# Performance work log

Hardware: AMD Instinct MI355X
Metric: run time of the kernel (lower is better)

Reference implementation:

```python
import jax, jax.numpy as jnp
import numpy as np

D_MODEL = 1024
NUM_HEADS = 16
HEAD_DIM = D_MODEL // NUM_HEADS
ROPE_BASE = 10000.0


def _rotate_half(x):
    x1, x2 = jnp.split(x, 2, axis=-1)
    return jnp.concatenate([-x2, x1], axis=-1)


def _rope_cache(seq_len, head_dim, dtype):
    half = head_dim // 2
    inv_freq = 1.0 / (ROPE_BASE ** (jnp.arange(half, dtype=jnp.float32) / float(half)))
    t = jnp.arange(seq_len, dtype=jnp.float32)
    freqs = t[:, None] * inv_freq[None, :]          # [s, half]
    emb = jnp.concatenate([freqs, freqs], axis=-1)   # [s, head_dim]
    cos = jnp.cos(emb)[None, None, :, :].astype(dtype)  # [1,1,s,d]
    sin = jnp.sin(emb)[None, None, :, :].astype(dtype)
    return cos, sin


def setup_inputs() -> dict:
    key = jax.random.key(0)
    k1, k2, k3 = jax.random.split(key, 3)
    b, s = 4, 2048
    x = jax.random.normal(k1, (b, s, D_MODEL), dtype=jnp.float32)
    mask = jnp.ones((b, s), dtype=jnp.float32)
    Wqkv = jax.random.normal(k2, (D_MODEL, 3 * D_MODEL), dtype=jnp.float32) * (D_MODEL ** -0.5)
    Wout = jax.random.normal(k3, (D_MODEL, D_MODEL), dtype=jnp.float32) * (D_MODEL ** -0.5)
    return {"x": x, "mask": mask, "Wqkv": Wqkv, "Wout": Wout}


def reference(x, mask, Wqkv, Wout):
    b, s, _ = x.shape
    qkv = x @ Wqkv                                   # [b,s,3*d_model]
    q, k, v = jnp.split(qkv, 3, axis=-1)

    def split_heads(t):
        return t.reshape(b, s, NUM_HEADS, HEAD_DIM).transpose(0, 2, 1, 3)  # [b,h,s,d]

    q, k, v = map(split_heads, (q, k, v))
    cos, sin = _rope_cache(s, HEAD_DIM, x.dtype)
    q = q * cos + _rotate_half(q) * sin
    k = k * cos + _rotate_half(k) * sin

    scale = HEAD_DIM ** -0.5
    logits = jnp.einsum('bhid,bhjd->bhij', q, k) * scale
    logits = logits + (1.0 - mask)[:, None, None, :] * -1e9
    attn = jax.nn.softmax(logits, axis=-1)
    out = jnp.einsum('bhij,bhjd->bhid', attn, v)     # [b,h,s,d]
    out = out.transpose(0, 2, 1, 3).reshape(b, s, D_MODEL)
    return out @ Wout
```

## Files before the change

### kernel.cpp

```cpp
#include <hip/hip_runtime.h>

typedef unsigned short u16;
typedef unsigned int u32;
typedef int i32x2 __attribute__((ext_vector_type(2)));
typedef float f32x4 __attribute__((ext_vector_type(4)));
typedef float f32x16 __attribute__((ext_vector_type(16)));
typedef __bf16 bf16x8 __attribute__((ext_vector_type(8)));
typedef unsigned short u16x8 __attribute__((ext_vector_type(8)));
typedef unsigned short u16x4 __attribute__((ext_vector_type(4)));
typedef unsigned int u32x4 __attribute__((ext_vector_type(4)));

#define S_ 2048
#define DM 1024

#define LDS_U32(p) ((__attribute__((address_space(3))) unsigned int*)(p))
#define GLB_U32(p) ((const __attribute__((address_space(1))) unsigned int*)(p))

__device__ __forceinline__ u16 f2bf(float f) {
    unsigned int u = __float_as_uint(f);
    u += 0x7fffu + ((u >> 16) & 1u);
    return (u16)(u >> 16);
}
__device__ __forceinline__ float bf2f(u16 s) {
    return __uint_as_float(((unsigned int)s) << 16);
}
__device__ __forceinline__ float fast_exp2(float x) {
#if __has_builtin(__builtin_amdgcn_exp2f)
    return __builtin_amdgcn_exp2f(x);
#else
    return __expf(x * 0.69314718056f);
#endif
}

__global__ __launch_bounds__(256) void f32_to_bf16_kernel(const float* __restrict__ in,
                                                          u16* __restrict__ o, int n) {
    int i = (blockIdx.x * 256 + threadIdx.x) << 2;
    if (i >= n) return;
    float4 f = *(const float4*)&in[i];
    u16x4 r;
    r[0] = f2bf(f.x); r[1] = f2bf(f.y); r[2] = f2bf(f.z); r[3] = f2bf(f.w);
    *(u16x4*)&o[i] = r;
}

__global__ __launch_bounds__(256) void transpose_w(const float* __restrict__ W,
                                                   u16* __restrict__ Wt, int K, int N) {
    __shared__ float tile[32][33];
    int nb = blockIdx.x << 5, kb = blockIdx.y << 5;
    int tx = threadIdx.x & 31, ty = threadIdx.x >> 5;
#pragma unroll
    for (int r = 0; r < 32; r += 8)
        tile[ty + r][tx] = W[(size_t)(kb + ty + r) * N + nb + tx];
    __syncthreads();
#pragma unroll
    for (int r = 0; r < 32; r += 8)
        Wt[(size_t)(nb + ty + r) * K + kb + tx] = f2bf(tile[tx][ty + r]);
}


#define ABLK(B, KK) ((B) * 24576 + (KK) * 4096)
#define BBLK(B, KK) ((B) * 24576 + 8192 + (KK) * 8192)

template <int MODE>
__global__ __launch_bounds__(512, 1) void gemm256(const u16* __restrict__ A,
                                                  const u16* __restrict__ Bt,
                                                  float* __restrict__ Cf,
                                                  u16* __restrict__ Qp, u16* __restrict__ Kp,
                                                  u16* __restrict__ Vtp,
                                                  int M, int N, int K) {
    __shared__ __align__(16) u16 lds[73728];
    const int tid = threadIdx.x, wave = tid >> 6, lane = tid & 63;
    const int Ntiles = N >> 8;
    const int cpx = gridDim.x >> 3;
    const int bid = (int)blockIdx.x;
    const int wg = (bid & 7) * cpx + (bid >> 3);
    const int mt = wg / Ntiles, nt = wg % Ntiles;
    const int m0 = mt << 7, n0 = nt << 8;
    const int wm = (wave >> 2) << 6, wn = (wave & 3) << 6;
    const int lr = lane & 15, lu = lane >> 4;

    const int NT = K >> 6;

    f32x4 acc[4][4] = {};

    const int srow0 = wave * 16 + (lane >> 2);
    const int scole = (((lane & 3) ^ ((lane >> 3) & 3)) << 3);

#define STAGE_A(BLK, KCOL)                                                                \
    {                                                                                     \
        const u16* src = &A[(size_t)(m0 + srow0) * K + (KCOL) + scole];                   \
        __builtin_amdgcn_global_load_lds(GLB_U32(src),                                    \
            LDS_U32(&lds[(BLK) + wave * 512]), 16, 0, 0);                                 \
    }
#define STAGE_B(BLK, KCOL)                                                                \
    {                                                                                     \
        _Pragma("unroll") for (int l = 0; l < 2; ++l) {                                   \
            const u16* src = &Bt[(size_t)(n0 + srow0 + l * 128) * K + (KCOL) + scole];    \
            __builtin_amdgcn_global_load_lds(GLB_U32(src),                                \
                LDS_U32(&lds[(BLK) + l * 4096 + wave * 512]), 16, 0, 0);                  \
        }                                                                                 \
    }

#define LDFRAG(BLK, ROW) \
    __builtin_bit_cast(bf16x8, *(const u16x8*)&lds[(BLK) + (ROW) * 32 + ((lu ^ (((ROW) >> 1) & 3)) << 3)])

#define PHASE(BUF, KK, SBUF, SKK, SKT)                                                    \
    {                                                                                     \
        _Pragma("unroll") for (int ii = 0; ii < 4; ++ii)                                  \
            af[ii] = LDFRAG(ABLK(BUF, KK), wm + ii * 16 + lr);                            \
        _Pragma("unroll") for (int j = 0; j < 4; ++j)                                     \
            bfv[j] = LDFRAG(BBLK(BUF, KK), wn + j * 16 + lr);                             \
        {                                                                                 \
            const int kcol = (((SKT) & (NT - 1)) << 6) + ((SKK) << 5);                    \
            STAGE_A(ABLK(SBUF, SKK), kcol);                                               \
            STAGE_B(BBLK(SBUF, SKK), kcol);                                               \
        }                                                                                 \
        asm volatile("s_barrier" ::: "memory");                                           \
        asm volatile("s_waitcnt lgkmcnt(0)" ::: "memory");                                \
        __builtin_amdgcn_sched_barrier(0);                                                \
        __builtin_amdgcn_s_setprio(1);                                                    \
        _Pragma("unroll") for (int ii = 0; ii < 4; ++ii)                                  \
            _Pragma("unroll") for (int j = 0; j < 4; ++j)                                 \
                acc[ii][j] = __builtin_amdgcn_mfma_f32_16x16x32_bf16(                     \
                    af[ii], bfv[j], acc[ii][j], 0, 0, 0);                                 \
        __builtin_amdgcn_s_setprio(0);                                                    \
        asm volatile("s_waitcnt vmcnt(9)" ::: "memory");                                  \
        asm volatile("s_barrier" ::: "memory");                                           \
    }

    STAGE_A(ABLK(0, 0), 0);
    STAGE_B(BBLK(0, 0), 0);
    STAGE_A(ABLK(0, 1), 32);
    STAGE_B(BBLK(0, 1), 32);
    STAGE_A(ABLK(1, 0), 64);
    STAGE_B(BBLK(1, 0), 64);
    STAGE_A(ABLK(1, 1), 96);
    STAGE_B(BBLK(1, 1), 96);
    asm volatile("s_waitcnt vmcnt(9)" ::: "memory");
    asm volatile("s_barrier" ::: "memory");

    int bt = 0, bs = 2;
    for (int t = 0; t < NT; ++t) {
        bf16x8 af[4], bfv[4];
        const int tn = t + 2;
        PHASE(bt, 0, bs, 0, tn);
        PHASE(bt, 1, bs, 1, tn);
        bt = (bt == 2) ? 0 : bt + 1;
        bs = (bs == 2) ? 0 : bs + 1;
    }

    if (MODE == 0) {
        const int t = (n0 + wn) >> 10;
        if (t < 2) {
            const float LN1E4_32 = 9.210340371976184f / 32.0f;
            const float invf0 = __expf(-(float)lr * LN1E4_32);
            const float invf1 = __expf(-(float)(lr + 16) * LN1E4_32);
#pragma unroll
            for (int i = 0; i < 4; ++i) {
                const int rbase = m0 + wm + (i << 4) + ((lane >> 4) << 2);
#pragma unroll
                for (int jj = 0; jj < 4; ++jj) {
                    const float s = (float)((rbase + jj) & (S_ - 1));
                    float sn0, c0, sn1, c1;
                    __sincosf(s * invf0, &sn0, &c0);
                    __sincosf(s * invf1, &sn1, &c1);
                    const float v0 = acc[i][0][jj], v1 = acc[i][1][jj];
                    const float v2 = acc[i][2][jj], v3 = acc[i][3][jj];
                    acc[i][0][jj] = v0 * c0 - v2 * sn0;
                    acc[i][2][jj] = v2 * c0 + v0 * sn0;
                    acc[i][1][jj] = v1 * c1 - v3 * sn1;
                    acc[i][3][jj] = v3 * c1 + v1 * sn1;
                }
            }
            u16* P = (t == 0) ? Qp : Kp;
#pragma unroll
            for (int i = 0; i < 4; ++i) {
#pragma unroll
                for (int j = 0; j < 4; ++j) {
                    int rbase = m0 + wm + (i << 4) + ((lane >> 4) << 2);
                    int col = n0 + wn + (j << 4) + lr;
                    int h = (col & 1023) >> 6, d = col & 63;
#pragma unroll
                    for (int jj = 0; jj < 4; ++jj) {
                        int row = rbase + jj;
                        int b = row >> 11, s = row & 2047;
                        P[((size_t)((b << 4) + h) * S_ + s) * 64 + d] = f2bf(acc[i][j][jj]);
                    }
                }
            }
        } else {
#pragma unroll
            for (int i = 0; i < 4; ++i) {
                const int rbase = m0 + wm + (i << 4) + ((lane >> 4) << 2);
                const int b = rbase >> 11, sb = rbase & 2047;
#pragma unroll
                for (int j = 0; j < 4; ++j) {
                    int col = n0 + wn + (j << 4) + lr;
                    int h = (col & 1023) >> 6, d = col & 63;
                    u16x4 pk;
#pragma unroll
                    for (int jj = 0; jj < 4; ++jj) pk[jj] = f2bf(acc[i][j][jj]);
                    *(u16x4*)&Vtp[((size_t)((b << 4) + h) * 64 + d) * S_ + sb] = pk;
                }
            }
        }
    } else {
#pragma unroll
        for (int i = 0; i < 4; ++i)
#pragma unroll
            for (int j = 0; j < 4; ++j) {
                int rbase = m0 + wm + (i << 4) + ((lane >> 4) << 2);
                int col = n0 + wn + (j << 4) + lr;
#pragma unroll
                for (int jj = 0; jj < 4; ++jj)
                    Cf[(size_t)(rbase + jj) * N + col] = acc[i][j][jj];
            }
    }
#undef PHASE
#undef LDFRAG
#undef STAGE_B
#undef STAGE_A
}

__device__ __forceinline__ void softmax_chain(f32x16* p, f32x16* acc, f32x16& accS,
                                              float& m_run, u32* wa, u32* wb,
                                              const float* madd_tile, bool hasmask,
                                              float* bcast_w, int c, int hi) {
    if (hasmask) {
#pragma unroll
        for (int tt = 0; tt < 2; ++tt)
#pragma unroll
            for (int rq = 0; rq < 4; ++rq) {
                float4 mf = *(const float4*)&madd_tile[tt * 32 + rq * 8 + hi * 4];
                p[tt][4 * rq + 0] += mf.x;
                p[tt][4 * rq + 1] += mf.y;
                p[tt][4 * rq + 2] += mf.z;
                p[tt][4 * rq + 3] += mf.w;
            }
    }

    float tm[16];
#pragma unroll
    for (int r = 0; r < 16; ++r) tm[r] = fmaxf(p[0][r], p[1][r]);
    float a0 = fmaxf(fmaxf(tm[0], tm[1]), tm[2]);
    float a1 = fmaxf(fmaxf(tm[3], tm[4]), tm[5]);
    float a2 = fmaxf(fmaxf(tm[6], tm[7]), tm[8]);
    float a3 = fmaxf(fmaxf(tm[9], tm[10]), tm[11]);
    float a4 = fmaxf(fmaxf(tm[12], tm[13]), tm[14]);
    float b0 = fmaxf(fmaxf(a0, a1), a2);
    float b1 = fmaxf(fmaxf(a3, a4), tm[15]);
    float mx = fmaxf(b0, b1);
    {
        i32x2 mm = __builtin_amdgcn_permlane32_swap(__float_as_int(mx), __float_as_int(mx), false, false);
        mx = fmaxf(__int_as_float(mm[0]), __int_as_float(mm[1]));
    }

    if (!__all(mx - m_run <= 8.0f)) {
        float mnew = fmaxf(m_run, mx);
        float alpha = fast_exp2(m_run - mnew);
        m_run = mnew;
        bcast_w[c] = alpha;
        float avf[16];
#pragma unroll
        for (int rq = 0; rq < 4; ++rq) {
            float4 t4 = *(const float4*)&bcast_w[rq * 8 + hi * 4];
            avf[4 * rq + 0] = t4.x; avf[4 * rq + 1] = t4.y;
            avf[4 * rq + 2] = t4.z; avf[4 * rq + 3] = t4.w;
        }
#pragma unroll
        for (int r = 0; r < 16; ++r) {
            acc[0][r] *= avf[r];
            acc[1][r] *= avf[r];
            accS[r]   *= avf[r];
        }
    }

#pragma unroll
    for (int tt = 0; tt < 2; ++tt)
#pragma unroll
        for (int r = 0; r < 16; ++r)
            p[tt][r] = fast_exp2(p[tt][r] - m_run);

#pragma unroll
    for (int tt = 0; tt < 2; ++tt)
#pragma unroll
        for (int rq = 0; rq < 4; ++rq) {
            float e0 = p[tt][4 * rq + 0], e1 = p[tt][4 * rq + 1];
            float e2 = p[tt][4 * rq + 2], e3 = p[tt][4 * rq + 3];
            u32 w0, w1;
            asm("v_cvt_pk_bf16_f32 %0, %1, %2" : "=v"(w0) : "v"(e0), "v"(e1));
            asm("v_cvt_pk_bf16_f32 %0, %1, %2" : "=v"(w1) : "v"(e2), "v"(e3));
            wa[4 * tt + rq] = w0;
            wb[4 * tt + rq] = w1;
        }
}

__global__ __launch_bounds__(256, 2) void attn_kernel(const u16* __restrict__ q,
                                                      const u16* __restrict__ k,
                                                      const u16* __restrict__ vt,
                                                      const float* __restrict__ mask,
                                                      u16* __restrict__ outp) {
    __shared__ __align__(16) u16 Kl[2][64 * 64];
    __shared__ __align__(16) u16 Vl[2][64 * 64];
    __shared__ float madd2[2][64];
    __shared__ float bcast[4][32];

    const int tid = threadIdx.x, wave = tid >> 6, lane = tid & 63;
    const int c = lane & 31, hi = lane >> 5, c7 = c & 7;
    const int bh = blockIdx.x & 63, qt = blockIdx.x >> 6;
    const int b = bh >> 4, h = bh & 15;
    const size_t base = (size_t)bh * (S_ * 64);
    const int qrowA = (qt << 8) + (wave << 5) + c;
    const int qrowB = qrowA + 128;

    const float QS = 0.18033688f;

    bf16x8 qfA[4], qfB[4];
#pragma unroll
    for (int j = 0; j < 4; ++j) {
        u16x8 rawA = *(const u16x8*)&q[base + (size_t)qrowA * 64 + j * 16 + hi * 8];
        u16x8 rawB = *(const u16x8*)&q[base + (size_t)qrowB * 64 + j * 16 + hi * 8];
        u16x8 scA, scB;
#pragma unroll
        for (int e = 0; e < 8; ++e) {
            scA[e] = f2bf(bf2f(rawA[e]) * QS);
            scB[e] = f2bf(bf2f(rawB[e]) * QS);
        }
        qfA[j] = __builtin_bit_cast(bf16x8, scA);
        qfB[j] = __builtin_bit_cast(bf16x8, scB);
    }

    u16x8 ou;
#pragma unroll
    for (int e = 0; e < 8; ++e) ou[e] = 0x3F80;
    const bf16x8 onesf = __builtin_bit_cast(bf16x8, ou);

    f32x16 accA[2] = {}, accB[2] = {};
    f32x16 accSA = {}, accSB = {};
    float m_runA = -1e30f, m_runB = -1e30f;

    const int sr = tid >> 2, su = (tid & 3) << 1;
    const int so0 = sr * 64 + ((su ^ (sr & 7)) << 3);
    const int so1 = sr * 64 + (((su + 1) ^ (sr & 7)) << 3);

    u16x8 kc0 = *(const u16x8*)&k[base + (size_t)sr * 64 + su * 8];
    u16x8 kc1 = *(const u16x8*)&k[base + (size_t)sr * 64 + su * 8 + 8];
    u16x8 vc0 = *(const u16x8*)&vt[base + (size_t)sr * S_ + su * 8];
    u16x8 vc1 = *(const u16x8*)&vt[base + (size_t)sr * S_ + su * 8 + 8];
    float mval = (tid < 64) ? mask[b * S_ + tid] : 1.0f;

    for (int t = 0; t < 32; ++t) {
        const int bi = t & 1;
        u16* Kb = &Kl[bi][0];
        u16* Vb = &Vl[bi][0];
        *(u16x8*)&Kb[so0] = kc0;
        *(u16x8*)&Kb[so1] = kc1;
        *(u16x8*)&Vb[so0] = vc0;
        *(u16x8*)&Vb[so1] = vc1;
        if (tid < 64) madd2[bi][tid] = (1.0f - mval) * -1.44269504e9f;
        if (t + 1 < 32) {
            const int kn = (t + 1) << 6;
            kc0 = *(const u16x8*)&k[base + (size_t)(kn + sr) * 64 + su * 8];
            kc1 = *(const u16x8*)&k[base + (size_t)(kn + sr) * 64 + su * 8 + 8];
            vc0 = *(const u16x8*)&vt[base + (size_t)sr * S_ + kn + su * 8];
            vc1 = *(const u16x8*)&vt[base + (size_t)sr * S_ + kn + su * 8 + 8];
            mval = (tid < 64) ? mask[b * S_ + kn + tid] : 1.0f;
        }
        __syncthreads();

        f32x16 pA[2] = {}, pB[2] = {};
        __builtin_amdgcn_s_setprio(1);
#pragma unroll
        for (int j = 0; j < 4; ++j) {
            const int uo = ((2 * j + hi) ^ c7) << 3;
            bf16x8 ka  = __builtin_bit_cast(bf16x8, *(const u16x8*)&Kb[c * 64 + uo]);
            bf16x8 kb2 = __builtin_bit_cast(bf16x8, *(const u16x8*)&Kb[(32 + c) * 64 + uo]);
            pA[0] = __builtin_amdgcn_mfma_f32_32x32x16_bf16(ka,  qfA[j], pA[0], 0, 0, 0);
            pA[1] = __builtin_amdgcn_mfma_f32_32x32x16_bf16(kb2, qfA[j], pA[1], 0, 0, 0);
            pB[0] = __builtin_amdgcn_mfma_f32_32x32x16_bf16(ka,  qfB[j], pB[0], 0, 0, 0);
            pB[1] = __builtin_amdgcn_mfma_f32_32x32x16_bf16(kb2, qfB[j], pB[1], 0, 0, 0);
        }
        __builtin_amdgcn_s_setprio(0);

        bool hasmask = __any(madd2[bi][lane] != 0.0f);

        u32 waA[8], wbA[8], waB[8], wbB[8];
        softmax_chain(pA, accA, accSA, m_runA, waA, wbA, &madd2[bi][0], hasmask, &bcast[wave][0], c, hi);
        softmax_chain(pB, accB, accSB, m_runB, waB, wbB, &madd2[bi][0], hasmask, &bcast[wave][0], c, hi);

        __builtin_amdgcn_s_setprio(1);
#pragma unroll
        for (int ks = 0; ks < 4; ++ks) {
            i32x2 raA = __builtin_amdgcn_permlane32_swap((int)waA[2 * ks], (int)waA[2 * ks + 1], false, false);
            i32x2 rbA = __builtin_amdgcn_permlane32_swap((int)wbA[2 * ks], (int)wbA[2 * ks + 1], false, false);
            i32x2 raB = __builtin_amdgcn_permlane32_swap((int)waB[2 * ks], (int)waB[2 * ks + 1], false, false);
            i32x2 rbB = __builtin_amdgcn_permlane32_swap((int)wbB[2 * ks], (int)wbB[2 * ks + 1], false, false);
            u32x4 pwA, pwB;
            pwA[0] = (u32)raA[0]; pwA[1] = (u32)rbA[0]; pwA[2] = (u32)raA[1]; pwA[3] = (u32)rbA[1];
            pwB[0] = (u32)raB[0]; pwB[1] = (u32)rbB[0]; pwB[2] = (u32)raB[1]; pwB[3] = (u32)rbB[1];
            bf16x8 pafA = __builtin_bit_cast(bf16x8, pwA);
            bf16x8 pafB = __builtin_bit_cast(bf16x8, pwB);
            accSA = __builtin_amdgcn_mfma_f32_32x32x16_bf16(pafA, onesf, accSA, 0, 0, 0);
            accSB = __builtin_amdgcn_mfma_f32_32x32x16_bf16(pafB, onesf, accSB, 0, 0, 0);
            const int uo = ((2 * ks + hi) ^ c7) << 3;
#pragma unroll
            for (int dt = 0; dt < 2; ++dt) {
                bf16x8 vf = __builtin_bit_cast(bf16x8,
                            *(const u16x8*)&Vb[(32 * dt + c) * 64 + uo]);
                accA[dt] = __builtin_amdgcn_mfma_f32_32x32x16_bf16(pafA, vf, accA[dt], 0, 0, 0);
                accB[dt] = __builtin_amdgcn_mfma_f32_32x32x16_bf16(pafB, vf, accB[dt], 0, 0, 0);
            }
        }
        __builtin_amdgcn_s_setprio(0);
    }

    {
        const size_t orow0 = (size_t)b * S_ + (qt << 8) + (wave << 5);
#pragma unroll
        for (int dt = 0; dt < 2; ++dt)
#pragma unroll
            for (int r = 0; r < 16; ++r) {
                int qr = (r & 3) + 8 * (r >> 2) + 4 * hi;
                outp[(orow0 + qr) * DM + h * 64 + dt * 32 + c] =
                    f2bf(accA[dt][r] * __builtin_amdgcn_rcpf(accSA[r]));
            }
    }
    {
        const size_t orow0 = (size_t)b * S_ + (qt << 8) + (wave << 5) + 128;
#pragma unroll
        for (int dt = 0; dt < 2; ++dt)
#pragma unroll
            for (int r = 0; r < 16; ++r) {
                int qr = (r & 3) + 8 * (r >> 2) + 4 * hi;
                outp[(orow0 + qr) * DM + h * 64 + dt * 32 + c] =
                    f2bf(accB[dt][r] * __builtin_amdgcn_rcpf(accSB[r]));
            }
    }
}

extern "C" void kernel_launch(void* const* d_in, const int* in_sizes, int n_in,
                              void* d_out, int out_size, void* d_ws, size_t ws_size,
                              hipStream_t stream) {
    const float* x    = (const float*)d_in[0];
    const float* mask = (const float*)d_in[1];
    const float* Wqkv = (const float*)d_in[2];
    const float* Wout = (const float*)d_in[3];
    float* out = (float*)d_out;
    char* ws = (char*)d_ws;
    const size_t MB = 1u << 20;
    u16* xb    = (u16*)(ws);
    u16* WqkvT = (u16*)(ws + 16 * MB);
    u16* WoutT = (u16*)(ws + 22 * MB);
    u16* qb    = (u16*)(ws + 24 * MB);
    u16* kb    = (u16*)(ws + 40 * MB);
    u16* vtb   = (u16*)(ws + 56 * MB);
    u16* ao    = xb;

    f32_to_bf16_kernel<<<8192, 256, 0, stream>>>(x, xb, 8192 * 1024);
    transpose_w<<<dim3(96, 32), 256, 0, stream>>>(Wqkv, WqkvT, 1024, 3072);
    transpose_w<<<dim3(32, 32), 256, 0, stream>>>(Wout, WoutT, 1024, 1024);
    gemm256<0><<<64 * 12, 512, 0, stream>>>(xb, WqkvT, nullptr, qb, kb, vtb, 8192, 3072, 1024);
    attn_kernel<<<512, 256, 0, stream>>>(qb, kb, vtb, mask, ao);
    gemm256<1><<<64 * 4, 512, 0, stream>>>(ao, WoutT, out, nullptr, nullptr, nullptr, 8192, 1024, 1024);
}
```

Baseline: 206.3 us.

## Double-buffer LDS fragment reads and fully unroll GEMM main loop

The GEMM main loop now reads the next phase's A/B fragments from LDS into a second register set while the MFMAs run on the current set, which removes the mid-phase barrier and lgkmcnt wait before the MFMAs. The K loop is fully unrolled into fixed-length macro cycles (12+12+8 phases), which hard-codes the triple-buffer indices and NT=16. The vmcnt threshold changes to 6 to match the new issue order. This is meant to hide LDS read latency behind MFMA work, at the cost of more registers and a fixed K length.

```diff
diff --git a/kernel.cpp b/kernel.cpp
--- a/kernel.cpp
+++ b/kernel.cpp
@@ -103,29 +103,54 @@
 #define LDFRAG(BLK, ROW) \
     __builtin_bit_cast(bf16x8, *(const u16x8*)&lds[(BLK) + (ROW) * 32 + ((lu ^ (((ROW) >> 1) & 3)) << 3)])
 
-#define PHASE(BUF, KK, SBUF, SKK, SKT)                                                    \
+#define READ(R, BUF, KK)                                                                  \
     {                                                                                     \
         _Pragma("unroll") for (int ii = 0; ii < 4; ++ii)                                  \
-            af[ii] = LDFRAG(ABLK(BUF, KK), wm + ii * 16 + lr);                            \
+            af##R[ii] = LDFRAG(ABLK(BUF, KK), wm + ii * 16 + lr);                         \
         _Pragma("unroll") for (int j = 0; j < 4; ++j)                                     \
-            bfv[j] = LDFRAG(BBLK(BUF, KK), wn + j * 16 + lr);                             \
-        {                                                                                 \
-            const int kcol = (((SKT) & (NT - 1)) << 6) + ((SKK) << 5);                    \
-            STAGE_A(ABLK(SBUF, SKK), kcol);                                               \
-            STAGE_B(BBLK(SBUF, SKK), kcol);                                               \
-        }                                                                                 \
-        asm volatile("s_barrier" ::: "memory");                                           \
-        asm volatile("s_waitcnt lgkmcnt(0)" ::: "memory");                                \
+            bfv##R[j] = LDFRAG(BBLK(BUF, KK), wn + j * 16 + lr);                          \
+    }
+
+#define PHASE(R, M, RBUF, RKK, SBUF, SKK, SKT)                                            \
+    {                                                                                     \
+        READ(R, RBUF, RKK);                                                               \
+        const int kcol = (((SKT) & (NT - 1)) << 6) + ((SKK) << 5);                        \
+        STAGE_A(ABLK(SBUF, SKK), kcol);                                                   \
+        STAGE_B(BBLK(SBUF, SKK), kcol);                                                   \
         __builtin_amdgcn_sched_barrier(0);                                                \
         __builtin_amdgcn_s_setprio(1);                                                    \
         _Pragma("unroll") for (int ii = 0; ii < 4; ++ii)                                  \
             _Pragma("unroll") for (int j = 0; j < 4; ++j)                                 \
                 acc[ii][j] = __builtin_amdgcn_mfma_f32_16x16x32_bf16(                     \
-                    af[ii], bfv[j], acc[ii][j], 0, 0, 0);                                 \
+                    af##M[ii], bfv##M[j], acc[ii][j], 0, 0, 0);                           \
         __builtin_amdgcn_s_setprio(0);                                                    \
-        asm volatile("s_waitcnt vmcnt(9)" ::: "memory");                                  \
+        asm volatile("s_waitcnt lgkmcnt(0)" ::: "memory");                                \
+        asm volatile("s_waitcnt vmcnt(6)" ::: "memory");                                  \
         asm volatile("s_barrier" ::: "memory");                                           \
     }
+
+#define CYCLE12(T0)                          \
+    PHASE(1, 0, 0, 1, 2, 0, (T0) + 2)       \
+    PHASE(0, 1, 1, 0, 2, 1, (T0) + 2)       \
+    PHASE(1, 0, 1, 1, 0, 0, (T0) + 3)       \
+    PHASE(0, 1, 2, 0, 0, 1, (T0) + 3)       \
+    PHASE(1, 0, 2, 1, 1, 0, (T0) + 4)       \
+    PHASE(0, 1, 0, 0, 1, 1, (T0) + 4)       \
+    PHASE(1, 0, 0, 1, 2, 0, (T0) + 5)       \
+    PHASE(0, 1, 1, 0, 2, 1, (T0) + 5)       \
+    PHASE(1, 0, 1, 1, 0, 0, (T0) + 6)       \
+    PHASE(0, 1, 2, 0, 0, 1, (T0) + 6)       \
+    PHASE(1, 0, 2, 1, 1, 0, (T0) + 7)       \
+    PHASE(0, 1, 0, 0, 1, 1, (T0) + 7)
+#define CYCLE8(T0)                           \
+    PHASE(1, 0, 0, 1, 2, 0, (T0) + 2)       \
+    PHASE(0, 1, 1, 0, 2, 1, (T0) + 2)       \
+    PHASE(1, 0, 1, 1, 0, 0, (T0) + 3)       \
+    PHASE(0, 1, 2, 0, 0, 1, (T0) + 3)       \
+    PHASE(1, 0, 2, 1, 1, 0, (T0) + 4)       \
+    PHASE(0, 1, 0, 0, 1, 1, (T0) + 4)       \
+    PHASE(1, 0, 0, 1, 2, 0, (T0) + 5)       \
+    PHASE(0, 1, 1, 0, 2, 1, (T0) + 5)
 
     STAGE_A(ABLK(0, 0), 0);
     STAGE_B(BBLK(0, 0), 0);
@@ -135,18 +160,17 @@
     STAGE_B(BBLK(1, 0), 64);
     STAGE_A(ABLK(1, 1), 96);
     STAGE_B(BBLK(1, 1), 96);
-    asm volatile("s_waitcnt vmcnt(9)" ::: "memory");
+    asm volatile("s_waitcnt vmcnt(6)" ::: "memory");
     asm volatile("s_barrier" ::: "memory");
 
-    int bt = 0, bs = 2;
-    for (int t = 0; t < NT; ++t) {
-        bf16x8 af[4], bfv[4];
-        const int tn = t + 2;
-        PHASE(bt, 0, bs, 0, tn);
-        PHASE(bt, 1, bs, 1, tn);
-        bt = (bt == 2) ? 0 : bt + 1;
-        bs = (bs == 2) ? 0 : bs + 1;
-    }
+    bf16x8 af0[4], bfv0[4], af1[4], bfv1[4];
+    READ(0, 0, 0);
+    asm volatile("s_waitcnt lgkmcnt(0)" ::: "memory");
+    __builtin_amdgcn_sched_barrier(0);
+
+    CYCLE12(0)
+    CYCLE12(6)
+    CYCLE8(12)
 
     if (MODE == 0) {
         const int t = (n0 + wn) >> 10;
@@ -215,7 +239,10 @@
                     Cf[(size_t)(rbase + jj) * N + col] = acc[i][j][jj];
             }
     }
+#undef CYCLE8
+#undef CYCLE12
 #undef PHASE
+#undef READ
 #undef LDFRAG
 #undef STAGE_B
 #undef STAGE_A
```

Result: no change. 207.2 us (+0.4%).
